# Kernel optimization log

Hardware: AMD Instinct MI355X
Metric: run time of the kernel (lower is better)

The kernel has to match this reference:

```python
import jax, jax.numpy as jnp
import numpy as np


def setup_inputs() -> dict:
    key = jax.random.key(0)
    kx, kf = jax.random.split(key)
    x = jax.random.normal(kx, (1, 3, 512, 512), dtype=jnp.float32)
    # per-pixel 9x9 kernels; normalize each to sum to 1 like a PSF
    kernel_field = jax.random.uniform(kf, (512, 512, 9, 9), dtype=jnp.float32)
    kernel_field = kernel_field / jnp.sum(kernel_field, axis=(-2, -1), keepdims=True)
    return {"x": x, "kernel_field": kernel_field}


def reference(x, kernel_field):
    """Spatially varying blur: out[b,c,h,w] = sum_{i,j} x_pad[b,c,h+i,w+j] * K[h,w,i,j].

    Equivalent to the torch unfold + einsum('bckhw,khw->bchw') but computed as a
    fused shift-multiply-accumulate over the kH*kW offsets, avoiding the
    (B,C,kH*kW,H,W) im2col blowup.
    """
    B, C, H, W = x.shape
    kH, kW = kernel_field.shape[2], kernel_field.shape[3]
    pad = kH // 2
    xp = jnp.pad(x, ((0, 0), (0, 0), (pad, pad), (pad, pad)), mode="reflect")
    out = jnp.zeros_like(x)
    for i in range(kH):          # small fixed loop over kernel taps (81)
        for j in range(kW):
            out = out + xp[:, :, i:i + H, j:j + W] * kernel_field[:, :, i, j]
    return out
```

## Files before the change

### kernel.cpp

```cpp
#include <hip/hip_runtime.h>
#include <stdint.h>

#define H 512
#define W 512
#define HW (H * W)
#define KT 81
#define PAD 4
#define SEGW 64

__device__ __forceinline__ int reflect_idx(int p) {
    if (p < 0) p = -p;
    if (p >= H) p = 2 * H - 2 - p;
    return p;
}

__global__ __launch_bounds__(192) void svblur_kernel(
    const float* __restrict__ x,
    const float* __restrict__ kf,
    float* __restrict__ out)
{
    __shared__ float wlds[SEGW * KT];

    const int tid = (int)threadIdx.x;
    const int l   = tid & 63;
    const int wv  = tid >> 6;
    const int bid = (int)blockIdx.x;
    const int h   = bid >> 3;
    const int w0  = (bid & 7) << 6;

    {
        const float4* ws = (const float4*)(kf + ((size_t)h * W + w0) * KT);
        float4* wd = (float4*)wlds;
#pragma unroll
        for (int it = 0; it < 7; ++it) {
            int idx = (wv * 7 + it) * 64 + l;
            if (idx < (SEGW * KT) / 4)
                wd[idx] = ws[idx];
        }
    }
    __syncthreads();

    int rgw[9];
#pragma unroll
    for (int j = 0; j < 9; ++j)
        rgw[j] = reflect_idx(w0 - PAD + l + j);

    const float* xc = x + (size_t)wv * HW;

    float xv[81];
#pragma unroll
    for (int i = 0; i < 9; ++i) {
        const float* row = xc + (size_t)reflect_idx(h - PAD + i) * W;
#pragma unroll
        for (int j = 0; j < 9; ++j)
            xv[i * 9 + j] = row[rgw[j]];
    }

    const float* wp = wlds + l * KT;
    float a0 = 0.f, a1 = 0.f, a2 = 0.f;
#pragma unroll
    for (int t = 0; t < 81; t += 3) {
        a0 = fmaf(xv[t],     wp[t],     a0);
        if (t + 1 < 81) a1 = fmaf(xv[t + 1], wp[t + 1], a1);
        if (t + 2 < 81) a2 = fmaf(xv[t + 2], wp[t + 2], a2);
    }

    out[(size_t)wv * HW + h * W + w0 + l] = a0 + a1 + a2;
}

extern "C" void kernel_launch(void* const* d_in, const int* in_sizes, int n_in,
                              void* d_out, int out_size, void* d_ws, size_t ws_size,
                              hipStream_t stream) {
    const float* x  = (const float*)d_in[0];
    const float* kf = (const float*)d_in[1];
    float* out = (float*)d_out;

    dim3 block(192);
    dim3 grid(H * (W / SEGW));
    svblur_kernel<<<grid, block, 0, stream>>>(x, kf, out);
}
```

Baseline: 25.53 us.

## Pre-pad input with reflection into workspace and use vector row loads

```diff
diff --git a/kernel.cpp b/kernel.cpp
--- a/kernel.cpp
+++ b/kernel.cpp
@@ -7,6 +7,11 @@
 #define KT 81
 #define PAD 4
 #define SEGW 64
+#define PW 520
+#define PPLANE (PW * PW)
+#define PADTOT (3 * PPLANE)
+
+typedef float f4u __attribute__((ext_vector_type(4), aligned(4)));
 
 __device__ __forceinline__ int reflect_idx(int p) {
     if (p < 0) p = -p;
@@ -14,8 +19,20 @@
     return p;
 }
 
+__global__ __launch_bounds__(256) void pad_kernel(
+    const float* __restrict__ x, float* __restrict__ xpad)
+{
+    int idx = blockIdx.x * 256 + threadIdx.x;
+    if (idx >= PADTOT) return;
+    int c   = idx / PPLANE;
+    int rem = idx - c * PPLANE;
+    int r   = rem / PW;
+    int col = rem - r * PW;
+    xpad[idx] = x[(size_t)c * HW + reflect_idx(r - PAD) * W + reflect_idx(col - PAD)];
+}
+
 __global__ __launch_bounds__(192) void svblur_kernel(
-    const float* __restrict__ x,
+    const float* __restrict__ xpad,
     const float* __restrict__ kf,
     float* __restrict__ out)
 {
@@ -40,29 +57,26 @@
     }
     __syncthreads();
 
-    int rgw[9];
-#pragma unroll
-    for (int j = 0; j < 9; ++j)
-        rgw[j] = reflect_idx(w0 - PAD + l + j);
+    const float* xbase = xpad + (size_t)wv * PPLANE + (size_t)h * PW + w0 + l;
+    const float* wp = wlds + l * KT;
 
-    const float* xc = x + (size_t)wv * HW;
-
-    float xv[81];
+    float a0 = 0.f, a1 = 0.f, a2 = 0.f;
 #pragma unroll
     for (int i = 0; i < 9; ++i) {
-        const float* row = xc + (size_t)reflect_idx(h - PAD + i) * W;
-#pragma unroll
-        for (int j = 0; j < 9; ++j)
-            xv[i * 9 + j] = row[rgw[j]];
-    }
-
-    const float* wp = wlds + l * KT;
-    float a0 = 0.f, a1 = 0.f, a2 = 0.f;
-#pragma unroll
-    for (int t = 0; t < 81; t += 3) {
-        a0 = fmaf(xv[t],     wp[t],     a0);
-        if (t + 1 < 81) a1 = fmaf(xv[t + 1], wp[t + 1], a1);
-        if (t + 2 < 81) a2 = fmaf(xv[t + 2], wp[t + 2], a2);
+        const float* rp = xbase + i * PW;
+        f4u A  = *(const f4u*)(rp);
+        f4u Bv = *(const f4u*)(rp + 4);
+        float Cv = rp[8];
+        const float* wr = wp + i * 9;
+        a0 = fmaf(A.x,  wr[0], a0);
+        a1 = fmaf(A.y,  wr[1], a1);
+        a2 = fmaf(A.z,  wr[2], a2);
+        a0 = fmaf(A.w,  wr[3], a0);
+        a1 = fmaf(Bv.x, wr[4], a1);
+        a2 = fmaf(Bv.y, wr[5], a2);
+        a0 = fmaf(Bv.z, wr[6], a0);
+        a1 = fmaf(Bv.w, wr[7], a1);
+        a2 = fmaf(Cv,   wr[8], a2);
     }
 
     out[(size_t)wv * HW + h * W + w0 + l] = a0 + a1 + a2;
@@ -73,9 +87,9 @@
                               hipStream_t stream) {
     const float* x  = (const float*)d_in[0];
     const float* kf = (const float*)d_in[1];
-    float* out = (float*)d_out;
+    float* out  = (float*)d_out;
+    float* xpad = (float*)d_ws;
 
-    dim3 block(192);
-    dim3 grid(H * (W / SEGW));
-    svblur_kernel<<<grid, block, 0, stream>>>(x, kf, out);
+    pad_kernel<<<(PADTOT + 255) / 256, 256, 0, stream>>>(x, xpad);
+    svblur_kernel<<<H * (W / SEGW), 192, 0, stream>>>(xpad, kf, out);
 }
```

Result: slower. 29.54 us (+15.7%).
